# Kernel optimization log

Hardware: AMD Instinct MI355X
Metric: run time of the kernel (lower is better)

## Reference

```python
import jax, jax.numpy as jnp
import numpy as np

EPS = 1e-6

def elu_feature_map(x):
    return jax.nn.elu(x) + 1.0

def setup_inputs() -> dict:
    key = jax.random.key(0)
    kq, kk, kv = jax.random.split(key, 3)
    N, L, S, H, D = 8, 8192, 8192, 8, 32
    return {
        "queries": jax.random.normal(kq, (N, L, H, D), dtype=jnp.float32),
        "keys": jax.random.normal(kk, (N, S, H, D), dtype=jnp.float32),
        "values": jax.random.normal(kv, (N, S, H, D), dtype=jnp.float32),
    }

def reference(queries, keys, values):
    # Linear (kernelized) attention, default path of MixAttention.forward
    Q = elu_feature_map(queries)            # [N,L,H,D]
    K = elu_feature_map(keys)               # [N,S,H,D]
    v_length = values.shape[1]
    vals = values / v_length                # [N,S,H,D]
    KV = jnp.einsum('nshd,nshv->nhdv', K, vals)          # [N,H,D,D]
    Z = 1.0 / (jnp.einsum('nlhd,nhd->nlh', Q, K.sum(axis=1)) + EPS)  # [N,L,H]
    out = jnp.einsum('nlhd,nhdv,nlh->nlhv', Q, KV, Z) * v_length     # [N,L,H,D]
    return out
```

## Files before the change

### kernel.cpp

```cpp
#include <hip/hip_runtime.h>


constexpr int N_ = 8, L_ = 8192, S_ = 8192, H_ = 8, D_ = 32;
constexpr int NH = N_ * H_;
constexpr int SPLIT = 32;
constexpr int CS = S_ / SPLIT;
constexpr int TS = 64;
constexpr int PART_STRIDE = D_ * D_ + D_;
constexpr int LCH = 512;
constexpr float EPS_ = 1e-6f;

__device__ __forceinline__ float fmap(float x) {
    return x > 0.0f ? x + 1.0f : __expf(x);
}

__global__ __launch_bounds__(256, 4) void lin_attn_phase1(
        const float* __restrict__ Kg, const float* __restrict__ Vg,
        float* __restrict__ part) {
    const int blk = blockIdx.x;
    const int nh = blk / SPLIT;
    const int sc = blk % SPLIT;
    const int n = nh / H_, h = nh % H_;
    const int t = threadIdx.x;
    const int g  = t >> 5;
    const int j  = t & 31;
    const int d0 = (j >> 3) << 3;
    const int v0 = (j & 7) << 2;
    const int srow = t >> 3;
    const int scol = (t & 7) << 2;

    __shared__ __align__(16) float smem[8 * 1024];
    __shared__ float ksum_sh[D_];
    float (*Kt)[D_] = (float(*)[D_])smem;
    float (*Vt)[D_] = (float(*)[D_])(smem + TS * D_);

    if (t < D_) ksum_sh[t] = 0.0f;

    float acc[8][4];
    #pragma unroll
    for (int a = 0; a < 8; ++a)
        #pragma unroll
        for (int b = 0; b < 4; ++b) acc[a][b] = 0.0f;
    float kp0 = 0.f, kp1 = 0.f, kp2 = 0.f, kp3 = 0.f;

    const size_t base = (size_t)n * S_ * H_ * D_ + (size_t)h * D_;
    const int s0 = sc * CS;
    for (int ss = 0; ss < CS; ss += TS) {
        const size_t o0 = base + (size_t)(s0 + ss + srow) * (H_ * D_) + scol;
        const size_t o1 = base + (size_t)(s0 + ss + srow + 32) * (H_ * D_) + scol;
        float4 k0 = *reinterpret_cast<const float4*>(Kg + o0);
        float4 k1 = *reinterpret_cast<const float4*>(Kg + o1);
        const float4 va = *reinterpret_cast<const float4*>(Vg + o0);
        const float4 vb = *reinterpret_cast<const float4*>(Vg + o1);
        k0.x = fmap(k0.x); k0.y = fmap(k0.y); k0.z = fmap(k0.z); k0.w = fmap(k0.w);
        k1.x = fmap(k1.x); k1.y = fmap(k1.y); k1.z = fmap(k1.z); k1.w = fmap(k1.w);
        kp0 += k0.x + k1.x; kp1 += k0.y + k1.y;
        kp2 += k0.z + k1.z; kp3 += k0.w + k1.w;
        __syncthreads();
        *reinterpret_cast<float4*>(&Kt[srow     ][scol]) = k0;
        *reinterpret_cast<float4*>(&Kt[srow + 32][scol]) = k1;
        *reinterpret_cast<float4*>(&Vt[srow     ][scol]) = va;
        *reinterpret_cast<float4*>(&Vt[srow + 32][scol]) = vb;
        __syncthreads();
        #pragma unroll
        for (int r = 0; r < 8; ++r) {
            const int row = (g << 3) + r;
            const float4 ka = *reinterpret_cast<const float4*>(&Kt[row][d0]);
            const float4 kb = *reinterpret_cast<const float4*>(&Kt[row][d0 + 4]);
            const float4 vv = *reinterpret_cast<const float4*>(&Vt[row][v0]);
            const float kd[8] = {ka.x, ka.y, ka.z, ka.w, kb.x, kb.y, kb.z, kb.w};
            const float vs[4] = {vv.x, vv.y, vv.z, vv.w};
            #pragma unroll
            for (int a = 0; a < 8; ++a)
                #pragma unroll
                for (int b = 0; b < 4; ++b)
                    acc[a][b] += kd[a] * vs[b];
        }
    }

    __syncthreads();
    float* red = smem;
    #pragma unroll
    for (int a = 0; a < 8; ++a) {
        const float4 w = make_float4(acc[a][0], acc[a][1], acc[a][2], acc[a][3]);
        *reinterpret_cast<float4*>(&red[(size_t)g * 1024 + (d0 + a) * D_ + v0]) = w;
    }
    atomicAdd(&ksum_sh[scol + 0], kp0);
    atomicAdd(&ksum_sh[scol + 1], kp1);
    atomicAdd(&ksum_sh[scol + 2], kp2);
    atomicAdd(&ksum_sh[scol + 3], kp3);
    __syncthreads();

    float* P = part + ((size_t)sc * NH + nh) * PART_STRIDE;
    const int i4 = t << 2;
    float4 s = make_float4(0.f, 0.f, 0.f, 0.f);
    #pragma unroll
    for (int g2 = 0; g2 < 8; ++g2) {
        const float4 rr = *reinterpret_cast<const float4*>(&red[(size_t)g2 * 1024 + i4]);
        s.x += rr.x; s.y += rr.y; s.z += rr.z; s.w += rr.w;
    }
    *reinterpret_cast<float4*>(&P[i4]) = s;
    if (t < D_) P[D_ * D_ + t] = ksum_sh[t];
}

__global__ __launch_bounds__(256) void lin_attn_reduce(
        const float* __restrict__ part, float* __restrict__ red) {
    const int i = blockIdx.x * 256 + threadIdx.x;
    if (i >= NH * PART_STRIDE) return;
    float s = 0.0f;
    #pragma unroll
    for (int sc = 0; sc < SPLIT; ++sc)
        s += part[(size_t)sc * (NH * PART_STRIDE) + i];
    red[i] = s;
}

__global__ __launch_bounds__(256) void lin_attn_phase2(
        const float* __restrict__ Qg, const float* __restrict__ red,
        float* __restrict__ outg) {
    constexpr int QTS = 32;
    constexpr int NLC = L_ / LCH;
    const int nh  = blockIdx.x / NLC;
    const int lcb = blockIdx.x % NLC;
    const int n = nh / H_, h = nh % H_;
    const int t = threadIdx.x;
    const int v  = t & 31;
    const int rb = t >> 5;
    const int r  = t >> 3;
    const int c  = (t & 7) << 2;

    __shared__ float Qt[QTS][D_];

    float kv[D_];
    float ks[D_];
    {
        const float* W = red + (size_t)nh * PART_STRIDE;
        #pragma unroll
        for (int d = 0; d < D_; ++d) kv[d] = W[d * D_ + v];
        #pragma unroll
        for (int d = 0; d < D_; ++d) ks[d] = W[D_ * D_ + d];
    }

    const size_t base = (size_t)n * L_ * H_ * D_ + (size_t)h * D_;
    const int l0 = lcb * LCH;
    for (int step = 0; step < LCH; step += QTS) {
        const float4 q4 = *reinterpret_cast<const float4*>(
            Qg + base + (size_t)(l0 + step + r) * (H_ * D_) + c);
        __syncthreads();
        float4 qf;
        qf.x = fmap(q4.x); qf.y = fmap(q4.y);
        qf.z = fmap(q4.z); qf.w = fmap(q4.w);
        *reinterpret_cast<float4*>(&Qt[r][c]) = qf;
        __syncthreads();
        #pragma unroll
        for (int rr = 0; rr < 4; ++rr) {
            const int row = (rr << 3) + rb;
            float acc = 0.0f, accz = 0.0f;
            #pragma unroll
            for (int d = 0; d < D_; ++d) {
                const float q = Qt[row][d];
                acc  += q * kv[d];
                accz += q * ks[d];
            }
            outg[base + (size_t)(l0 + step + row) * (H_ * D_) + v] =
                acc / (accz + EPS_);
        }
    }
}

extern "C" void kernel_launch(void* const* d_in, const int* in_sizes, int n_in,
                              void* d_out, int out_size, void* d_ws, size_t ws_size,
                              hipStream_t stream) {
    const float* Q = (const float*)d_in[0];
    const float* K = (const float*)d_in[1];
    const float* V = (const float*)d_in[2];
    float* out  = (float*)d_out;
    float* part = (float*)d_ws;
    float* red  = part + (size_t)SPLIT * NH * PART_STRIDE;

    lin_attn_phase1<<<NH * SPLIT, 256, 0, stream>>>(K, V, part);
    lin_attn_reduce<<<(NH * PART_STRIDE + 255) / 256, 256, 0, stream>>>(part, red);
    lin_attn_phase2<<<NH * (L_ / LCH), 256, 0, stream>>>(Q, red, out);
}
```

Before: 92.65 us.

## Compute phase1 KV outer products directly from global loads, dropping shared staging

Phase1 no longer stages K and V tiles through shared memory with two barriers per tile. Each lane now loads its own K slice and V slice straight from global memory, and the two half-waves' partial products are combined with cross-lane shuffles. This removes the per-tile LDS traffic and syncs, drops the ksum atomics, and raises the occupancy hint to 8 blocks per CU. In exchange, lanes re-read V rows from global, which relies on cache hits. Phase2 also reads Q from shared memory as float4 instead of scalars.

```diff
diff --git a/kernel.cpp b/kernel.cpp
--- a/kernel.cpp
+++ b/kernel.cpp
@@ -5,7 +5,6 @@
 constexpr int NH = N_ * H_;
 constexpr int SPLIT = 32;
 constexpr int CS = S_ / SPLIT;
-constexpr int TS = 64;
 constexpr int PART_STRIDE = D_ * D_ + D_;
 constexpr int LCH = 512;
 constexpr float EPS_ = 1e-6f;
@@ -14,7 +13,7 @@
     return x > 0.0f ? x + 1.0f : __expf(x);
 }
 
-__global__ __launch_bounds__(256, 4) void lin_attn_phase1(
+__global__ __launch_bounds__(256, 8) void lin_attn_phase1(
         const float* __restrict__ Kg, const float* __restrict__ Vg,
         float* __restrict__ part) {
     const int blk = blockIdx.x;
@@ -22,85 +21,83 @@
     const int sc = blk % SPLIT;
     const int n = nh / H_, h = nh % H_;
     const int t = threadIdx.x;
-    const int g  = t >> 5;
-    const int j  = t & 31;
-    const int d0 = (j >> 3) << 3;
-    const int v0 = (j & 7) << 2;
-    const int srow = t >> 3;
-    const int scol = (t & 7) << 2;
+    const int w = t >> 6;
+    const int j = t & 63;
+    const int half = j >> 5;
+    const int jj = j & 31;
+    const int d0 = (jj & 7) << 2;
+    const int v0 = (jj >> 3) << 3;
 
-    __shared__ __align__(16) float smem[8 * 1024];
-    __shared__ float ksum_sh[D_];
-    float (*Kt)[D_] = (float(*)[D_])smem;
-    float (*Vt)[D_] = (float(*)[D_])(smem + TS * D_);
+    __shared__ __align__(16) float red[4][1024];
+    __shared__ __align__(16) float ksum_red[4][32];
 
-    if (t < D_) ksum_sh[t] = 0.0f;
-
-    float acc[8][4];
+    float acc[4][8];
     #pragma unroll
-    for (int a = 0; a < 8; ++a)
+    for (int a = 0; a < 4; ++a)
         #pragma unroll
-        for (int b = 0; b < 4; ++b) acc[a][b] = 0.0f;
-    float kp0 = 0.f, kp1 = 0.f, kp2 = 0.f, kp3 = 0.f;
+        for (int b = 0; b < 8; ++b) acc[a][b] = 0.0f;
+    float kp[4] = {0.f, 0.f, 0.f, 0.f};
 
     const size_t base = (size_t)n * S_ * H_ * D_ + (size_t)h * D_;
+    const float* Kp = Kg + base;
+    const float* Vp = Vg + base;
     const int s0 = sc * CS;
-    for (int ss = 0; ss < CS; ss += TS) {
-        const size_t o0 = base + (size_t)(s0 + ss + srow) * (H_ * D_) + scol;
-        const size_t o1 = base + (size_t)(s0 + ss + srow + 32) * (H_ * D_) + scol;
-        float4 k0 = *reinterpret_cast<const float4*>(Kg + o0);
-        float4 k1 = *reinterpret_cast<const float4*>(Kg + o1);
-        const float4 va = *reinterpret_cast<const float4*>(Vg + o0);
-        const float4 vb = *reinterpret_cast<const float4*>(Vg + o1);
-        k0.x = fmap(k0.x); k0.y = fmap(k0.y); k0.z = fmap(k0.z); k0.w = fmap(k0.w);
-        k1.x = fmap(k1.x); k1.y = fmap(k1.y); k1.z = fmap(k1.z); k1.w = fmap(k1.w);
-        kp0 += k0.x + k1.x; kp1 += k0.y + k1.y;
-        kp2 += k0.z + k1.z; kp3 += k0.w + k1.w;
-        __syncthreads();
-        *reinterpret_cast<float4*>(&Kt[srow     ][scol]) = k0;
-        *reinterpret_cast<float4*>(&Kt[srow + 32][scol]) = k1;
-        *reinterpret_cast<float4*>(&Vt[srow     ][scol]) = va;
-        *reinterpret_cast<float4*>(&Vt[srow + 32][scol]) = vb;
-        __syncthreads();
+
+    int row = s0 + (w << 1) + half;
+    for (int b = 0; b < CS / 8; ++b, row += 8) {
+        const size_t off = (size_t)row * (H_ * D_);
+        const float4 kq = *reinterpret_cast<const float4*>(Kp + off + d0);
+        const float4 va = *reinterpret_cast<const float4*>(Vp + off + v0);
+        const float4 vb = *reinterpret_cast<const float4*>(Vp + off + v0 + 4);
+        float kd[4];
+        kd[0] = fmap(kq.x); kd[1] = fmap(kq.y);
+        kd[2] = fmap(kq.z); kd[3] = fmap(kq.w);
+        kp[0] += kd[0]; kp[1] += kd[1]; kp[2] += kd[2]; kp[3] += kd[3];
+        const float vs[8] = {va.x, va.y, va.z, va.w, vb.x, vb.y, vb.z, vb.w};
         #pragma unroll
-        for (int r = 0; r < 8; ++r) {
-            const int row = (g << 3) + r;
-            const float4 ka = *reinterpret_cast<const float4*>(&Kt[row][d0]);
-            const float4 kb = *reinterpret_cast<const float4*>(&Kt[row][d0 + 4]);
-            const float4 vv = *reinterpret_cast<const float4*>(&Vt[row][v0]);
-            const float kd[8] = {ka.x, ka.y, ka.z, ka.w, kb.x, kb.y, kb.z, kb.w};
-            const float vs[4] = {vv.x, vv.y, vv.z, vv.w};
+        for (int a = 0; a < 4; ++a)
             #pragma unroll
-            for (int a = 0; a < 8; ++a)
-                #pragma unroll
-                for (int b = 0; b < 4; ++b)
-                    acc[a][b] += kd[a] * vs[b];
-        }
+            for (int bb = 0; bb < 8; ++bb)
+                acc[a][bb] += kd[a] * vs[bb];
     }
 
-    __syncthreads();
-    float* red = smem;
     #pragma unroll
-    for (int a = 0; a < 8; ++a) {
-        const float4 w = make_float4(acc[a][0], acc[a][1], acc[a][2], acc[a][3]);
-        *reinterpret_cast<float4*>(&red[(size_t)g * 1024 + (d0 + a) * D_ + v0]) = w;
+    for (int a = 0; a < 4; ++a)
+        #pragma unroll
+        for (int bb = 0; bb < 8; ++bb)
+            acc[a][bb] += __shfl_xor(acc[a][bb], 32);
+    #pragma unroll
+    for (int a = 0; a < 4; ++a) kp[a] += __shfl_xor(kp[a], 32);
+
+    if (j < 32) {
+        #pragma unroll
+        for (int a = 0; a < 4; ++a) {
+            *reinterpret_cast<float4*>(&red[w][(d0 + a) * D_ + v0]) =
+                make_float4(acc[a][0], acc[a][1], acc[a][2], acc[a][3]);
+            *reinterpret_cast<float4*>(&red[w][(d0 + a) * D_ + v0 + 4]) =
+                make_float4(acc[a][4], acc[a][5], acc[a][6], acc[a][7]);
+        }
+        if (j < 8)
+            *reinterpret_cast<float4*>(&ksum_red[w][j << 2]) =
+                make_float4(kp[0], kp[1], kp[2], kp[3]);
     }
-    atomicAdd(&ksum_sh[scol + 0], kp0);
-    atomicAdd(&ksum_sh[scol + 1], kp1);
-    atomicAdd(&ksum_sh[scol + 2], kp2);
-    atomicAdd(&ksum_sh[scol + 3], kp3);
     __syncthreads();
 
     float* P = part + ((size_t)sc * NH + nh) * PART_STRIDE;
     const int i4 = t << 2;
     float4 s = make_float4(0.f, 0.f, 0.f, 0.f);
     #pragma unroll
-    for (int g2 = 0; g2 < 8; ++g2) {
-        const float4 rr = *reinterpret_cast<const float4*>(&red[(size_t)g2 * 1024 + i4]);
+    for (int w2 = 0; w2 < 4; ++w2) {
+        const float4 rr = *reinterpret_cast<const float4*>(&red[w2][i4]);
         s.x += rr.x; s.y += rr.y; s.z += rr.z; s.w += rr.w;
     }
     *reinterpret_cast<float4*>(&P[i4]) = s;
-    if (t < D_) P[D_ * D_ + t] = ksum_sh[t];
+    if (t < D_) {
+        float ks = 0.f;
+        #pragma unroll
+        for (int w2 = 0; w2 < 4; ++w2) ks += ksum_red[w2][t];
+        P[D_ * D_ + t] = ks;
+    }
 }
 
 __global__ __launch_bounds__(256) void lin_attn_reduce(
@@ -128,7 +125,7 @@
     const int r  = t >> 3;
     const int c  = (t & 7) << 2;
 
-    __shared__ float Qt[QTS][D_];
+    __shared__ __align__(16) float Qt[QTS][D_];
 
     float kv[D_];
     float ks[D_];
@@ -156,10 +153,12 @@
             const int row = (rr << 3) + rb;
             float acc = 0.0f, accz = 0.0f;
             #pragma unroll
-            for (int d = 0; d < D_; ++d) {
-                const float q = Qt[row][d];
-                acc  += q * kv[d];
-                accz += q * ks[d];
+            for (int d4 = 0; d4 < 8; ++d4) {
+                const float4 q = *reinterpret_cast<const float4*>(&Qt[row][d4 << 2]);
+                acc  += q.x * kv[(d4 << 2) + 0] + q.y * kv[(d4 << 2) + 1]
+                      + q.z * kv[(d4 << 2) + 2] + q.w * kv[(d4 << 2) + 3];
+                accz += q.x * ks[(d4 << 2) + 0] + q.y * ks[(d4 << 2) + 1]
+                      + q.z * ks[(d4 << 2) + 2] + q.w * ks[(d4 << 2) + 3];
             }
             outg[base + (size_t)(l0 + step + row) * (H_ * D_) + v] =
                 acc / (accz + EPS_);
```

Result: slower. 125.8 us (+35.8%).
